# Kernel tuning notes

Measured on AMD Instinct MI355X. Metric: run time of the kernel, lower is better.

Reference implementation:

```python
import jax, jax.numpy as jnp
import numpy as np

N_NODES = 100000
N_EDGES = 1000000  # even: first half = 'in' direction, second half = 'out' (inverse) direction
H = 128
N_REL = 200        # num_relations (for rel_labels embedding)
N_RELG = 100       # num_rel_graph; edge_type in [0, 2*N_RELG)
N_GRAPHS = 256
N_CLS = 2


def _glorot(key, shape):
    s = (6.0 / (shape[0] + shape[1])) ** 0.5
    return jax.random.uniform(key, shape, jnp.float32, -s, s)


def setup_inputs() -> dict:
    key = jax.random.key(0)
    ks = jax.random.split(key, 32)
    inp = {}
    inp['x'] = jax.random.normal(ks[0], (N_NODES, H), jnp.float32)
    inp['edge_index'] = jax.random.randint(ks[1], (2, N_EDGES), 0, N_NODES)
    inp['edge_type'] = jax.random.randint(ks[2], (N_EDGES,), 0, 2 * N_RELG)
    inp['batch'] = jnp.sort(jax.random.randint(ks[3], (N_NODES,), 0, N_GRAPHS))
    inp['rel_labels'] = jax.random.randint(ks[4], (N_GRAPHS,), 0, N_REL)
    inp['drop_prob'] = 0  # eval mode -> dropout is identity
    # learned parameters
    inp['rel_emb_table'] = jax.random.normal(ks[5], (N_REL, H), jnp.float32)
    inp['rel_graph_emb'] = _glorot(ks[6], (N_RELG, H))
    i = 7
    for l in (1, 2, 3):
        for nm in ('w_in', 'w_out', 'w_loop', 'w_rel'):
            inp[f'{nm}{l}'] = _glorot(ks[i], (H, H)); i += 1
        inp[f'loop_rel{l}'] = _glorot(ks[i], (1, H)); i += 1
        inp[f'b{l}'] = jnp.zeros((H,), jnp.float32)
    inp['lin_w'] = _glorot(ks[i], (2 * H, N_CLS))
    inp['lin_b'] = jnp.zeros((N_CLS,), jnp.float32)
    return inp


def _conv(x, edge_index, edge_type, rel, w_in, w_out, w_loop, w_rel, loop_rel, b):
    """CompGCNConv with 'sub' composition, tanh activation (BN/dropout identity in eval)."""
    n = x.shape[0]
    rel_all = jnp.concatenate([rel, loop_rel], axis=0)  # append loop relation
    half = edge_index.shape[1] // 2

    def direction(idx, etyp, w):
        src, dst = idx[0], idx[1]
        # norm as in CompGCN: deg over row(src), norm = deg_inv[row]*deg_inv[col]
        deg = jax.ops.segment_sum(jnp.ones(src.shape[0], x.dtype), src, num_segments=n)
        dinv = jnp.where(deg > 0, deg ** -0.5, 0.0)
        norm = dinv[src] * dinv[dst]                      # [E/2]
        msg = ((x[src] - rel_all[etyp]) @ w) * norm[:, None]  # gather-compose-transform
        return jax.ops.segment_sum(msg, dst, num_segments=n)  # scatter-add

    in_res = direction(edge_index[:, :half], edge_type[:half], w_in)
    out_res = direction(edge_index[:, half:], edge_type[half:], w_out)
    loop_res = (x - rel_all[-1]) @ w_loop
    out = (in_res + out_res + loop_res) * (1.0 / 3.0) + b
    return jnp.tanh(out), (rel_all @ w_rel)[:-1]


def reference(x, rel_emb_table, rel_graph_emb,
              w_in1, w_out1, w_loop1, w_rel1, loop_rel1, b1,
              w_in2, w_out2, w_loop2, w_rel2, loop_rel2, b2,
              w_in3, w_out3, w_loop3, w_rel3, loop_rel3, b3,
              lin_w, lin_b, edge_index, edge_type, batch, rel_labels, drop_prob):
    rel_embs = rel_emb_table[rel_labels]                   # [G, H]
    r = jnp.concatenate([rel_graph_emb, -rel_graph_emb], axis=0)  # [2*N_RELG, H]
    x, r = _conv(x, edge_index, edge_type, r, w_in1, w_out1, w_loop1, w_rel1, loop_rel1, b1)
    x = jax.nn.relu(x)
    x, r = _conv(x, edge_index, edge_type, r, w_in2, w_out2, w_loop2, w_rel2, loop_rel2, b2)
    x = jax.nn.relu(x)
    x, r = _conv(x, edge_index, edge_type, r, w_in3, w_out3, w_loop3, w_rel3, loop_rel3, b3)
    # global mean pool over graphs
    sums = jax.ops.segment_sum(x, batch, num_segments=N_GRAPHS)
    cnt = jax.ops.segment_sum(jnp.ones(batch.shape[0], x.dtype), batch, num_segments=N_GRAPHS)
    x = sums / jnp.maximum(cnt, 1.0)[:, None]              # [G, H]
    x = jnp.concatenate([x, rel_embs], axis=1)             # [G, 2H]
    # dropout identity (eval); final linear
    return x @ lin_w + lin_b                               # [G, 2]
```

## Files before the change

### kernel.cpp

```cpp
#include <hip/hip_runtime.h>
#include <hip/hip_bf16.h>
#include <math.h>

#define N_NODES 100000
#define N_EDGES 1000000
#define HALF_E  500000
#define H       128
#define NG      256
#define RELROWS 201
#define NH      (N_NODES * H)
#define SCAN_NB 98
#define XPITCH  136
#define MMB     64

typedef __attribute__((ext_vector_type(8))) short bf16x8;
typedef __attribute__((ext_vector_type(4))) float f32x4;
typedef __attribute__((ext_vector_type(2))) float f32x2;

__device__ __forceinline__ float bflo(unsigned p) { return __uint_as_float(p << 16); }
__device__ __forceinline__ float bfhi(unsigned p) { return __uint_as_float(p & 0xffff0000u); }
__device__ __forceinline__ unsigned packbf2(float a, float b) {
    unsigned ua = __float_as_uint(a), ub = __float_as_uint(b);
    ua = (ua + 0x7fffu + ((ua >> 16) & 1u)) >> 16;
    ub = (ub + 0x7fffu + ((ub >> 16) & 1u)) >> 16;
    return ua | (ub << 16);
}

__device__ __forceinline__ float fp8_to_f32(unsigned v) {
    unsigned s = (v & 0x80u) << 24;
    float m = __uint_as_float((v & 0x7fu) << 20) * 0x1p+120f;
    return __uint_as_float(__float_as_uint(m) | s);
}

#if __has_builtin(__builtin_amdgcn_cvt_pk_f32_fp8)
__device__ __forceinline__ f32x2 f8pair(unsigned short p) {
    return __builtin_amdgcn_cvt_pk_f32_fp8((int)(unsigned)p, false);
}
#else
__device__ __forceinline__ f32x2 f8pair(unsigned short p) {
    f32x2 r;
    r.x = fp8_to_f32(p & 0xffu);
    r.y = fp8_to_f32((p >> 8) & 0xffu);
    return r;
}
#endif

#if __has_builtin(__builtin_amdgcn_cvt_pk_fp8_f32)
__device__ __forceinline__ unsigned short packfp8_2(float a, float b) {
    int v = __builtin_amdgcn_cvt_pk_fp8_f32(a, b, 0, false);
    return (unsigned short)(v & 0xffff);
}
#else
__device__ __forceinline__ unsigned fp8_enc1(float x) {
    float ax = fabsf(x);
    ax = fminf(ax, 448.f);
    unsigned sgn = (__float_as_uint(x) >> 24) & 0x80u;
    float sc = ax * 0x1p-120f;
    unsigned b = __float_as_uint(sc);
    if (b < 0x00080000u) return sgn;
    unsigned r = b + 0x7ffffu + ((b >> 20) & 1u);
    return sgn | (r >> 20);
}
__device__ __forceinline__ unsigned short packfp8_2(float a, float b) {
    return (unsigned short)(fp8_enc1(a) | (fp8_enc1(b) << 8));
}
#endif

__global__ void deg_hist_kernel(const int* __restrict__ ei, float* deg_in, float* deg_out,
                                int* __restrict__ cnt_dst) {
    int e = blockIdx.x * 256 + threadIdx.x;
    if (e >= N_EDGES) return;
    int src = ei[e];
    int dst = ei[N_EDGES + e];
    if (e < HALF_E) atomicAdd(deg_in + src, 1.0f);
    else            atomicAdd(deg_out + src, 1.0f);
    atomicAdd(cnt_dst + dst, 1);
}

__global__ __launch_bounds__(1024) void scan1_kernel(const int* __restrict__ cnt,
                                                     int* __restrict__ excl,
                                                     int* __restrict__ bsum,
                                                     float* deg_in, float* deg_out) {
    __shared__ int ps[1024];
    int t = threadIdx.x;
    int i = blockIdx.x * 1024 + t;
    if (i < N_NODES) {
        float d = deg_in[i];  deg_in[i]  = d > 0.f ? rsqrtf(d) : 0.f;
        d = deg_out[i];       deg_out[i] = d > 0.f ? rsqrtf(d) : 0.f;
    }
    int v = (i < N_NODES) ? cnt[i] : 0;
    ps[t] = v;
    __syncthreads();
    for (int off = 1; off < 1024; off <<= 1) {
        int u = (t >= off) ? ps[t - off] : 0;
        __syncthreads();
        ps[t] += u;
        __syncthreads();
    }
    if (i < N_NODES) excl[i] = ps[t] - v;
    if (t == 1023) bsum[blockIdx.x] = ps[t];
}

__global__ __launch_bounds__(128) void scan2_kernel(const int* __restrict__ bsum,
                                                    int* __restrict__ boff,
                                                    int* __restrict__ rowptr,
                                                    const int* __restrict__ batch,
                                                    float* __restrict__ cnt_g) {
    __shared__ int ps[128];
    int t = threadIdx.x;
    for (int g = t; g < NG; g += 128) {
        int lo = 0, hi = N_NODES;
        while (lo < hi) { int mid = (lo + hi) >> 1; if (batch[mid] < g) lo = mid + 1; else hi = mid; }
        int start = lo;
        lo = 0; hi = N_NODES;
        while (lo < hi) { int mid = (lo + hi) >> 1; if (batch[mid] < g + 1) lo = mid + 1; else hi = mid; }
        cnt_g[g] = (float)(lo - start);
    }
    int v = (t < SCAN_NB) ? bsum[t] : 0;
    ps[t] = v;
    __syncthreads();
    for (int off = 1; off < 128; off <<= 1) {
        int u = (t >= off) ? ps[t - off] : 0;
        __syncthreads();
        ps[t] += u;
        __syncthreads();
    }
    if (t < SCAN_NB) boff[t] = ps[t] - v;
    if (t == 127) rowptr[N_NODES] = ps[t];
}

__global__ __launch_bounds__(1024) void scan3_kernel(const int* __restrict__ excl,
                                                     const int* __restrict__ boff,
                                                     int* __restrict__ rowptr,
                                                     int* __restrict__ rfill) {
    int t = threadIdx.x;
    int i = blockIdx.x * 1024 + t;
    if (i >= N_NODES) return;
    int r = excl[i] + boff[blockIdx.x];
    rowptr[i] = r;
    rfill[i] = r;
}

__global__ void fill_kernel(const int* __restrict__ ei, const int* __restrict__ etype,
                            const float* __restrict__ dinv_in, const float* __restrict__ dinv_out,
                            int* __restrict__ rfill, int2* __restrict__ csr_mn) {
    int e = blockIdx.x * 256 + threadIdx.x;
    if (e >= N_EDGES) return;
    int s = ei[e], d = ei[N_EDGES + e];
    int t = etype[e];
    bool isin = (e < HALF_E);
    const float* dv = isin ? dinv_in : dinv_out;
    float nv = dv[s] * dv[d];
    int j = atomicAdd(rfill + d, 1);
    int src2 = s + (isin ? 0 : N_NODES);
    int typ2 = t + (isin ? 0 : 200);
    csr_mn[j] = make_int2(src2 | (typ2 << 18), __float_as_int(nv));
}

__global__ void rel_mm_kernel(const float* __restrict__ rge, const float* __restrict__ loop_rel,
                              int layer,
                              const float* __restrict__ wIn, const float* __restrict__ wOut,
                              const float* __restrict__ wRel, const float* __restrict__ wLoop,
                              unsigned short* __restrict__ RWf8, float* __restrict__ rbuf,
                              float* __restrict__ lwl) {
    __shared__ float a[H];
    int i = blockIdx.x, j = threadIdx.x;
    float v;
    if (i == 200)        v = loop_rel[j];
    else if (layer == 1) v = (i < 100) ? rge[i * H + j] : -rge[(i - 100) * H + j];
    else                 v = rbuf[i * H + j];
    a[j] = v;
    __syncthreads();
    float s_in = 0.f, s_out = 0.f, s_rel = 0.f, s_loop = 0.f;
    for (int k = 0; k < H; k++) {
        float av = a[k];
        s_in  += av * wIn [k * H + j];
        s_out += av * wOut[k * H + j];
        s_rel += av * wRel[k * H + j];
        s_loop += av * wLoop[k * H + j];
    }
    float in_n  = __shfl_xor(s_in, 1);
    float out_n = __shfl_xor(s_out, 1);
    if (i < 200) {
        if ((j & 1) == 0) {
            RWf8[i * 64 + (j >> 1)]         = packfp8_2(s_in, in_n);
            RWf8[(200 + i) * 64 + (j >> 1)] = packfp8_2(s_out, out_n);
        }
        rbuf[i * H + j] = s_rel;
    }
    if (i == 200) lwl[j] = s_loop;
}

struct WPtrs { const float* p[9]; };
__global__ __launch_bounds__(256) void wpack_kernel(WPtrs wp, unsigned short* __restrict__ Bp) {
    int iw = blockIdx.y;
    const float* W = wp.p[iw];
    unsigned short* out = Bp + (size_t)iw * 16384;
    int t = blockIdx.x * 256 + threadIdx.x;
    int nt = t >> 8, kk = (t >> 6) & 3, lane = t & 63;
    int n = nt * 16 + (lane & 15);
    int k0 = kk * 32 + (lane >> 4) * 8;
    unsigned p[4];
    for (int j = 0; j < 4; j++)
        p[j] = packbf2(W[(k0 + 2 * j) * H + n], W[(k0 + 2 * j + 1) * H + n]);
    *(uint4*)(out + ((size_t)(nt * 4 + kk) * 64 + lane) * 8) = make_uint4(p[0], p[1], p[2], p[3]);
}

__global__ __launch_bounds__(256) void mm_mfma_kernel(const float* __restrict__ Xf,
                                                      const unsigned short* __restrict__ Xh,
                                                      int xf32,
                                                      const unsigned short* __restrict__ Bpack,
                                                      const float* __restrict__ lwl,
                                                      unsigned short* __restrict__ QRf8,
                                                      unsigned short* __restrict__ Sb) {
    __shared__ unsigned short xt[MMB * XPITCH];
    int tid = threadIdx.x;
    int row0 = blockIdx.x * MMB;
    int nrows = min(MMB, N_NODES - row0);
    if (xf32) {
        for (int t = 0; t < 8; t++) {
            int idx = tid + t * 256;
            int r = idx >> 5, c4 = (idx & 31) * 4;
            if (r < nrows) {
                float4 v = *(const float4*)(Xf + (size_t)(row0 + r) * H + c4);
                *(uint2*)(xt + r * XPITCH + c4) = make_uint2(packbf2(v.x, v.y), packbf2(v.z, v.w));
            }
        }
    } else {
        for (int t = 0; t < 4; t++) {
            int idx = tid + t * 256;
            int r = idx >> 4, c8 = (idx & 15) * 8;
            if (r < nrows)
                *(uint4*)(xt + r * XPITCH + c8) = *(const uint4*)(Xh + (size_t)(row0 + r) * H + c8);
        }
    }
    __syncthreads();

    int wave = tid >> 6, lane = tid & 63;
    int m0w = wave * 16;
    int q = lane >> 4, ml = lane & 15;
    bf16x8 afrag[4];
    for (int kk = 0; kk < 4; kk++)
        afrag[kk] = *(const bf16x8*)(xt + (m0w + ml) * XPITCH + kk * 32 + q * 8);
    __syncthreads();

    if (m0w + 16 > nrows) return;

    unsigned short* stg = xt + wave * 2176;
    unsigned* stg32 = (unsigned*)stg;
    uint4* stg4 = (uint4*)stg;
    int grow0 = row0 + m0w;

    for (int w = 0; w < 3; w++) {
        for (int nt = 0; nt < 8; nt++) {
            const unsigned short* bp = Bpack + (((size_t)(w * 8 + nt) * 4) * 64 + lane) * 8;
            f32x4 acc = {0.f, 0.f, 0.f, 0.f};
            for (int kk = 0; kk < 4; kk++) {
                bf16x8 bfrag = *(const bf16x8*)(bp + (size_t)kk * 512);
                acc = __builtin_amdgcn_mfma_f32_16x16x32_bf16(afrag[kk], bfrag, acc, 0, 0, 0);
            }
            if (w < 2) {
                #pragma unroll
                for (int reg = 0; reg < 4; reg++) {
                    float v = acc[reg];
                    float vn = __shfl_xor(v, 1);
                    if ((lane & 1) == 0)
                        stg[(q * 4 + reg) * 64 + nt * 8 + (ml >> 1)] = packfp8_2(v, vn);
                }
            } else {
                float sub = lwl[nt * 16 + ml];
                #pragma unroll
                for (int reg = 0; reg < 4; reg++) {
                    float v = acc[reg] - sub;
                    float vn = __shfl_xor(v, 1);
                    if ((lane & 1) == 0)
                        stg32[(q * 4 + reg) * 64 + nt * 8 + (ml >> 1)] = packbf2(v, vn);
                }
            }
        }
        if (w < 2) {
            size_t rbase = (w == 0) ? 0 : (size_t)N_NODES;
            uint4* dst = (uint4*)QRf8 + (rbase + grow0) * 8;
            dst[lane]      = stg4[lane];
            dst[lane + 64] = stg4[lane + 64];
        } else {
            uint4* dst = (uint4*)Sb + (size_t)grow0 * 16;
            #pragma unroll
            for (int i = 0; i < 4; i++)
                dst[lane + 64 * i] = stg4[lane + 64 * i];
        }
    }
}

__global__ __launch_bounds__(256, 8) void gather_kernel(const int* __restrict__ rowptr,
                                                        const int2* __restrict__ csr_mn,
                                                        const unsigned short* __restrict__ QRf8,
                                                        const unsigned short* __restrict__ RWf8,
                                                        const float* __restrict__ b,
                                                        unsigned* __restrict__ Sb,
                                                        const int* __restrict__ batch,
                                                        float* __restrict__ pool, int mode) {
    int v = blockIdx.x * 4 + (threadIdx.x >> 6);
    if (v >= N_NODES) return;
    int lane = threadIdx.x & 63;
    int c = lane * 2;
    int jb = rowptr[v], je = rowptr[v + 1];
    unsigned sv = Sb[(size_t)v * 64 + lane];
    float ax = bflo(sv), ay = bfhi(sv);
    int j = jb;
    for (; j + 7 < je; j += 8) {
        int2 mn[8];
        #pragma unroll
        for (int k = 0; k < 8; k++) mn[k] = csr_mn[j + k];
        unsigned short q[8], r[8];
        #pragma unroll
        for (int k = 0; k < 8; k++) {
            q[k] = QRf8[(size_t)(mn[k].x & 0x3FFFF) * 64 + lane];
            r[k] = RWf8[(size_t)((unsigned)mn[k].x >> 18) * 64 + lane];
        }
        #pragma unroll
        for (int k = 0; k < 8; k++) {
            float n = __int_as_float(mn[k].y);
            f32x2 dq = f8pair(q[k]);
            f32x2 dr = f8pair(r[k]);
            ax += (dq.x - dr.x) * n;
            ay += (dq.y - dr.y) * n;
        }
    }
    for (; j + 1 < je; j += 2) {
        int2 mn0 = csr_mn[j], mn1 = csr_mn[j + 1];
        unsigned short q0 = QRf8[(size_t)(mn0.x & 0x3FFFF) * 64 + lane];
        unsigned short r0 = RWf8[(size_t)((unsigned)mn0.x >> 18) * 64 + lane];
        unsigned short q1 = QRf8[(size_t)(mn1.x & 0x3FFFF) * 64 + lane];
        unsigned short r1 = RWf8[(size_t)((unsigned)mn1.x >> 18) * 64 + lane];
        float n0 = __int_as_float(mn0.y), n1 = __int_as_float(mn1.y);
        f32x2 dq0 = f8pair(q0), dr0 = f8pair(r0);
        f32x2 dq1 = f8pair(q1), dr1 = f8pair(r1);
        ax += (dq0.x - dr0.x) * n0; ay += (dq0.y - dr0.y) * n0;
        ax += (dq1.x - dr1.x) * n1; ay += (dq1.y - dr1.y) * n1;
    }
    if (j < je) {
        int2 mn0 = csr_mn[j];
        float n0 = __int_as_float(mn0.y);
        unsigned short q0 = QRf8[(size_t)(mn0.x & 0x3FFFF) * 64 + lane];
        unsigned short r0 = RWf8[(size_t)((unsigned)mn0.x >> 18) * 64 + lane];
        f32x2 dq0 = f8pair(q0), dr0 = f8pair(r0);
        ax += (dq0.x - dr0.x) * n0; ay += (dq0.y - dr0.y) * n0;
    }
    float v0 = tanhf(ax * (1.f / 3.f) + b[c]);
    float v1 = tanhf(ay * (1.f / 3.f) + b[c + 1]);
    if (mode == 0) {
        v0 = fmaxf(v0, 0.f); v1 = fmaxf(v1, 0.f);
        Sb[(size_t)v * 64 + lane] = packbf2(v0, v1);
    } else {
        int g = batch[v];
        atomicAdd(pool + g * H + c,     v0);
        atomicAdd(pool + g * H + c + 1, v1);
    }
}

__global__ void final_kernel(const float* __restrict__ pool, const float* __restrict__ cnt,
                             const float* __restrict__ rel_table, const int* __restrict__ rel_labels,
                             const float* __restrict__ lin_w, const float* __restrict__ lin_b,
                             float* __restrict__ out) {
    int g = blockIdx.x;
    int lane = threadIdx.x;
    float inv = 1.f / fmaxf(cnt[g], 1.f);
    const float* rrow = rel_table + (size_t)rel_labels[g] * H;
    float p0 = 0.f, p1 = 0.f;
    for (int c = lane; c < H; c += 64) {
        float m = pool[g * H + c] * inv;
        p0 += m * lin_w[c * 2 + 0];
        p1 += m * lin_w[c * 2 + 1];
        float rv = rrow[c];
        p0 += rv * lin_w[(H + c) * 2 + 0];
        p1 += rv * lin_w[(H + c) * 2 + 1];
    }
    for (int off = 32; off; off >>= 1) {
        p0 += __shfl_down(p0, off);
        p1 += __shfl_down(p1, off);
    }
    if (lane == 0) {
        out[g * 2 + 0] = p0 + lin_b[0];
        out[g * 2 + 1] = p1 + lin_b[1];
    }
}

extern "C" void kernel_launch(void* const* d_in, const int* in_sizes, int n_in,
                              void* d_out, int out_size, void* d_ws, size_t ws_size,
                              hipStream_t stream) {
    const float* x          = (const float*)d_in[0];
    const int*   ei         = (const int*)  d_in[1];
    const int*   etype      = (const int*)  d_in[2];
    const int*   batch      = (const int*)  d_in[3];
    const int*   rel_labels = (const int*)  d_in[4];
    const float* rel_table  = (const float*)d_in[6];
    const float* rge        = (const float*)d_in[7];
    const float* lin_w      = (const float*)d_in[26];
    const float* lin_b      = (const float*)d_in[27];
    float* out = (float*)d_out;

    float* ws       = (float*)d_ws;
    float* dinv_in  = ws;
    float* dinv_out = dinv_in + N_NODES;
    float* pool     = dinv_out + N_NODES;
    float* cnt      = pool + NG * H;
    float* rbuf     = cnt + NG;
    float* lwl      = rbuf + 200 * H;
    int*   rowptr   = (int*)(lwl + 3 * H);
    int*   rfill    = rowptr + N_NODES + 4;
    int*   cnt_dst  = rfill + N_NODES;
    int*   excl     = cnt_dst + N_NODES;
    int*   bsum     = excl + N_NODES;
    int*   boff     = bsum + 100;
    int2*  csr_mn   = (int2*)(boff + 100);
    unsigned short* QRf8 = (unsigned short*)(csr_mn + N_EDGES);
    unsigned* Sb    = (unsigned*)(QRf8 + (size_t)2 * N_NODES * 64);
    unsigned short* RWf8 = (unsigned short*)(Sb + (size_t)N_NODES * 64);
    unsigned short* Bpack = RWf8 + (size_t)3 * 400 * 64;

    hipMemsetAsync(dinv_in, 0, (size_t)(2 * N_NODES + NG * H + NG) * sizeof(float), stream);
    hipMemsetAsync(cnt_dst, 0, (size_t)N_NODES * sizeof(int), stream);

    deg_hist_kernel<<<(N_EDGES + 255) / 256, 256, 0, stream>>>(ei, dinv_in, dinv_out, cnt_dst);
    scan1_kernel   <<<SCAN_NB, 1024, 0, stream>>>(cnt_dst, excl, bsum, dinv_in, dinv_out);
    scan2_kernel   <<<1, 128, 0, stream>>>(bsum, boff, rowptr, batch, cnt);
    scan3_kernel   <<<SCAN_NB, 1024, 0, stream>>>(excl, boff, rowptr, rfill);
    fill_kernel    <<<(N_EDGES + 255) / 256, 256, 0, stream>>>(ei, etype, dinv_in, dinv_out,
                                                               rfill, csr_mn);

    WPtrs wp;
    for (int l = 0; l < 3; l++) {
        wp.p[l * 3 + 0] = (const float*)d_in[8 + 6 * l + 0];
        wp.p[l * 3 + 1] = (const float*)d_in[8 + 6 * l + 1];
        wp.p[l * 3 + 2] = (const float*)d_in[8 + 6 * l + 2];
    }
    wpack_kernel<<<dim3(8, 9), 256, 0, stream>>>(wp, Bpack);

    for (int l = 0; l < 3; l++) {
        const float* wIn   = (const float*)d_in[8 + 6 * l + 0];
        const float* wOut  = (const float*)d_in[8 + 6 * l + 1];
        const float* wLoop = (const float*)d_in[8 + 6 * l + 2];
        const float* wRel  = (const float*)d_in[8 + 6 * l + 3];
        const float* lrel  = (const float*)d_in[8 + 6 * l + 4];
        rel_mm_kernel<<<RELROWS, H, 0, stream>>>(rge, lrel, l + 1, wIn, wOut, wRel, wLoop,
                                                 RWf8 + (size_t)l * 400 * 64,
                                                 rbuf, lwl + l * H);
    }

    int mm_grid = (N_NODES + MMB - 1) / MMB;
    for (int l = 0; l < 3; l++) {
        const float* bl = (const float*)d_in[8 + 6 * l + 5];
        mm_mfma_kernel<<<mm_grid, 256, 0, stream>>>(x, (const unsigned short*)Sb, (l == 0) ? 1 : 0,
                                                    Bpack + (size_t)l * 3 * 16384, lwl + l * H,
                                                    QRf8, (unsigned short*)Sb);
        gather_kernel<<<N_NODES / 4, 256, 0, stream>>>(rowptr, csr_mn,
                                                       QRf8, RWf8 + (size_t)l * 400 * 64, bl,
                                                       Sb, batch, pool, (l == 2) ? 1 : 0);
    }

    final_kernel<<<NG, 64, 0, stream>>>(pool, cnt, rel_table, rel_labels, lin_w, lin_b, out);
}
```

Measured before the change: 697.1 us.

## Aggregate composed features before the weight transform, then fuse in/out/loop matmuls

The per-layer order changes from transform-then-aggregate to aggregate-then-transform. The gather kernel now reads a single fp8 copy of the node features (N rows instead of 2N precomputed in/out projections), subtracts bf16 relation embeddings, and accumulates separate in- and out-direction sums into bf16 buffers. A new combine kernel then runs MFMA over the in, out and self-loop inputs into one accumulator, and applies bias, tanh, relu and pooling in its epilogue. This halves the randomly gathered table size so it caches better, at the cost of writing and re-reading two extra N×H bf16 aggregate buffers per layer.

Result: slower. 948.4 us (+36.1%).

```diff
diff --git a/kernel.cpp b/kernel.cpp
--- a/kernel.cpp
+++ b/kernel.cpp
@@ -8,7 +8,6 @@
 #define H       128
 #define NG      256
 #define RELROWS 201
-#define NH      (N_NODES * H)
 #define SCAN_NB 98
 #define XPITCH  136
 #define MMB     64
@@ -31,20 +30,15 @@
     float m = __uint_as_float((v & 0x7fu) << 20) * 0x1p+120f;
     return __uint_as_float(__float_as_uint(m) | s);
 }
-
 #if __has_builtin(__builtin_amdgcn_cvt_pk_f32_fp8)
 __device__ __forceinline__ f32x2 f8pair(unsigned short p) {
     return __builtin_amdgcn_cvt_pk_f32_fp8((int)(unsigned)p, false);
 }
 #else
 __device__ __forceinline__ f32x2 f8pair(unsigned short p) {
-    f32x2 r;
-    r.x = fp8_to_f32(p & 0xffu);
-    r.y = fp8_to_f32((p >> 8) & 0xffu);
-    return r;
+    f32x2 r; r.x = fp8_to_f32(p & 0xffu); r.y = fp8_to_f32((p >> 8) & 0xffu); return r;
 }
 #endif
-
 #if __has_builtin(__builtin_amdgcn_cvt_pk_fp8_f32)
 __device__ __forceinline__ unsigned short packfp8_2(float a, float b) {
     int v = __builtin_amdgcn_cvt_pk_fp8_f32(a, b, 0, false);
@@ -152,16 +146,21 @@
     const float* dv = isin ? dinv_in : dinv_out;
     float nv = dv[s] * dv[d];
     int j = atomicAdd(rfill + d, 1);
-    int src2 = s + (isin ? 0 : N_NODES);
-    int typ2 = t + (isin ? 0 : 200);
-    csr_mn[j] = make_int2(src2 | (typ2 << 18), __float_as_int(nv));
+    int m = s | (t << 17) | (isin ? 0 : (1 << 25));
+    csr_mn[j] = make_int2(m, __float_as_int(nv));
+}
+
+__global__ void xcvt_kernel(const float* __restrict__ x, unsigned short* __restrict__ Xf8) {
+    int id = blockIdx.x * 256 + threadIdx.x;
+    if (id >= N_NODES * 64) return;
+    float2 v = *(const float2*)(x + (size_t)id * 2);
+    Xf8[id] = packfp8_2(v.x, v.y);
 }
 
 __global__ void rel_mm_kernel(const float* __restrict__ rge, const float* __restrict__ loop_rel,
                               int layer,
-                              const float* __restrict__ wIn, const float* __restrict__ wOut,
                               const float* __restrict__ wRel, const float* __restrict__ wLoop,
-                              unsigned short* __restrict__ RWf8, float* __restrict__ rbuf,
+                              unsigned* __restrict__ relb, float* __restrict__ rbuf,
                               float* __restrict__ lwl) {
     __shared__ float a[H];
     int i = blockIdx.x, j = threadIdx.x;
@@ -171,23 +170,16 @@
     else                 v = rbuf[i * H + j];
     a[j] = v;
     __syncthreads();
-    float s_in = 0.f, s_out = 0.f, s_rel = 0.f, s_loop = 0.f;
+    float vn = __shfl_xor(v, 1);
+    if (i < 200 && (j & 1) == 0)
+        relb[i * 64 + (j >> 1)] = packbf2(v, vn);
+    float s_rel = 0.f, s_loop = 0.f;
     for (int k = 0; k < H; k++) {
         float av = a[k];
-        s_in  += av * wIn [k * H + j];
-        s_out += av * wOut[k * H + j];
-        s_rel += av * wRel[k * H + j];
+        s_rel  += av * wRel [k * H + j];
         s_loop += av * wLoop[k * H + j];
     }
-    float in_n  = __shfl_xor(s_in, 1);
-    float out_n = __shfl_xor(s_out, 1);
-    if (i < 200) {
-        if ((j & 1) == 0) {
-            RWf8[i * 64 + (j >> 1)]         = packfp8_2(s_in, in_n);
-            RWf8[(200 + i) * 64 + (j >> 1)] = packfp8_2(s_out, out_n);
-        }
-        rbuf[i * H + j] = s_rel;
-    }
+    if (i < 200)  rbuf[i * H + j] = s_rel;
     if (i == 200) lwl[j] = s_loop;
 }
 
@@ -206,24 +198,91 @@
     *(uint4*)(out + ((size_t)(nt * 4 + kk) * 64 + lane) * 8) = make_uint4(p[0], p[1], p[2], p[3]);
 }
 
-__global__ __launch_bounds__(256) void mm_mfma_kernel(const float* __restrict__ Xf,
-                                                      const unsigned short* __restrict__ Xh,
+__global__ __launch_bounds__(256, 8) void gather_kernel(const int* __restrict__ rowptr,
+                                                        const int2* __restrict__ csr_mn,
+                                                        const unsigned short* __restrict__ Xf8,
+                                                        const unsigned* __restrict__ RELb,
+                                                        unsigned* __restrict__ AGGi,
+                                                        unsigned* __restrict__ AGGo) {
+    int v = blockIdx.x * 4 + (threadIdx.x >> 6);
+    if (v >= N_NODES) return;
+    int lane = threadIdx.x & 63;
+    int jb = rowptr[v], je = rowptr[v + 1];
+    float aix = 0.f, aiy = 0.f, aox = 0.f, aoy = 0.f;
+    int j = jb;
+    for (; j + 7 < je; j += 8) {
+        int2 mn[8];
+        #pragma unroll
+        for (int k = 0; k < 8; k++) mn[k] = csr_mn[j + k];
+        unsigned short xq[8]; unsigned rl[8];
+        #pragma unroll
+        for (int k = 0; k < 8; k++) {
+            xq[k] = Xf8[(size_t)(mn[k].x & 0x1FFFF) * 64 + lane];
+            rl[k] = RELb[((mn[k].x >> 17) & 0xFF) * 64 + lane];
+        }
+        #pragma unroll
+        for (int k = 0; k < 8; k++) {
+            float n = __int_as_float(mn[k].y);
+            f32x2 dx = f8pair(xq[k]);
+            float vx = dx.x - bflo(rl[k]);
+            float vy = dx.y - bfhi(rl[k]);
+            bool dir = (mn[k].x >> 25) & 1;
+            float ni = dir ? 0.f : n, no = dir ? n : 0.f;
+            aix += vx * ni; aiy += vy * ni;
+            aox += vx * no; aoy += vy * no;
+        }
+    }
+    for (; j < je; j++) {
+        int2 mn0 = csr_mn[j];
+        float n = __int_as_float(mn0.y);
+        unsigned short xq = Xf8[(size_t)(mn0.x & 0x1FFFF) * 64 + lane];
+        unsigned rl = RELb[((mn0.x >> 17) & 0xFF) * 64 + lane];
+        f32x2 dx = f8pair(xq);
+        float vx = dx.x - bflo(rl);
+        float vy = dx.y - bfhi(rl);
+        bool dir = (mn0.x >> 25) & 1;
+        float ni = dir ? 0.f : n, no = dir ? n : 0.f;
+        aix += vx * ni; aiy += vy * ni;
+        aox += vx * no; aoy += vy * no;
+    }
+    AGGi[(size_t)v * 64 + lane] = packbf2(aix, aiy);
+    AGGo[(size_t)v * 64 + lane] = packbf2(aox, aoy);
+}
+
+__global__ __launch_bounds__(256) void combine_kernel(const float* __restrict__ Xf,
+                                                      const unsigned* __restrict__ Xh,
                                                       int xf32,
+                                                      const unsigned* __restrict__ AGGi,
+                                                      const unsigned* __restrict__ AGGo,
                                                       const unsigned short* __restrict__ Bpack,
                                                       const float* __restrict__ lwl,
-                                                      unsigned short* __restrict__ QRf8,
-                                                      unsigned short* __restrict__ Sb) {
-    __shared__ unsigned short xt[MMB * XPITCH];
+                                                      const float* __restrict__ bvec,
+                                                      unsigned short* __restrict__ Xf8_out,
+                                                      unsigned* __restrict__ Xh_out,
+                                                      const int* __restrict__ batch,
+                                                      float* __restrict__ pool, int mode) {
+    __shared__ unsigned short ti[MMB * XPITCH];
+    __shared__ unsigned short to[MMB * XPITCH];
+    __shared__ unsigned short tx[MMB * XPITCH];
     int tid = threadIdx.x;
     int row0 = blockIdx.x * MMB;
     int nrows = min(MMB, N_NODES - row0);
+
+    for (int t = 0; t < 4; t++) {
+        int idx = tid + t * 256;
+        int r = idx >> 4, c8 = (idx & 15) * 8;
+        if (r < nrows) {
+            *(uint4*)(ti + r * XPITCH + c8) = *(const uint4*)((const unsigned short*)AGGi + (size_t)(row0 + r) * H + c8);
+            *(uint4*)(to + r * XPITCH + c8) = *(const uint4*)((const unsigned short*)AGGo + (size_t)(row0 + r) * H + c8);
+        }
+    }
     if (xf32) {
         for (int t = 0; t < 8; t++) {
             int idx = tid + t * 256;
             int r = idx >> 5, c4 = (idx & 31) * 4;
             if (r < nrows) {
                 float4 v = *(const float4*)(Xf + (size_t)(row0 + r) * H + c4);
-                *(uint2*)(xt + r * XPITCH + c4) = make_uint2(packbf2(v.x, v.y), packbf2(v.z, v.w));
+                *(uint2*)(tx + r * XPITCH + c4) = make_uint2(packbf2(v.x, v.y), packbf2(v.z, v.w));
             }
         }
     } else {
@@ -231,7 +290,7 @@
             int idx = tid + t * 256;
             int r = idx >> 4, c8 = (idx & 15) * 8;
             if (r < nrows)
-                *(uint4*)(xt + r * XPITCH + c8) = *(const uint4*)(Xh + (size_t)(row0 + r) * H + c8);
+                *(uint4*)(tx + r * XPITCH + c8) = *(const uint4*)((const unsigned short*)Xh + (size_t)(row0 + r) * H + c8);
         }
     }
     __syncthreads();
@@ -239,123 +298,69 @@
     int wave = tid >> 6, lane = tid & 63;
     int m0w = wave * 16;
     int q = lane >> 4, ml = lane & 15;
-    bf16x8 afrag[4];
-    for (int kk = 0; kk < 4; kk++)
-        afrag[kk] = *(const bf16x8*)(xt + (m0w + ml) * XPITCH + kk * 32 + q * 8);
+    bf16x8 fi[4], fo[4], fx[4];
+    for (int kk = 0; kk < 4; kk++) {
+        fi[kk] = *(const bf16x8*)(ti + (m0w + ml) * XPITCH + kk * 32 + q * 8);
+        fo[kk] = *(const bf16x8*)(to + (m0w + ml) * XPITCH + kk * 32 + q * 8);
+        fx[kk] = *(const bf16x8*)(tx + (m0w + ml) * XPITCH + kk * 32 + q * 8);
+    }
     __syncthreads();
 
     if (m0w + 16 > nrows) return;
 
-    unsigned short* stg = xt + wave * 2176;
-    unsigned* stg32 = (unsigned*)stg;
-    uint4* stg4 = (uint4*)stg;
     int grow0 = row0 + m0w;
-
-    for (int w = 0; w < 3; w++) {
-        for (int nt = 0; nt < 8; nt++) {
-            const unsigned short* bp = Bpack + (((size_t)(w * 8 + nt) * 4) * 64 + lane) * 8;
-            f32x4 acc = {0.f, 0.f, 0.f, 0.f};
-            for (int kk = 0; kk < 4; kk++) {
-                bf16x8 bfrag = *(const bf16x8*)(bp + (size_t)kk * 512);
-                acc = __builtin_amdgcn_mfma_f32_16x16x32_bf16(afrag[kk], bfrag, acc, 0, 0, 0);
-            }
-            if (w < 2) {
-                #pragma unroll
-                for (int reg = 0; reg < 4; reg++) {
-                    float v = acc[reg];
-                    float vn = __shfl_xor(v, 1);
-                    if ((lane & 1) == 0)
-                        stg[(q * 4 + reg) * 64 + nt * 8 + (ml >> 1)] = packfp8_2(v, vn);
-                }
-            } else {
-                float sub = lwl[nt * 16 + ml];
-                #pragma unroll
-                for (int reg = 0; reg < 4; reg++) {
-                    float v = acc[reg] - sub;
-                    float vn = __shfl_xor(v, 1);
-                    if ((lane & 1) == 0)
-                        stg32[(q * 4 + reg) * 64 + nt * 8 + (ml >> 1)] = packbf2(v, vn);
+    int grow_base = grow0 + q * 4;
+    unsigned short* stg8 = ti + wave * 1024;
+    unsigned* stgh = (unsigned*)to + wave * 1024;
+
+    int gmap[4];
+    if (mode == 1) {
+        #pragma unroll
+        for (int reg = 0; reg < 4; reg++) gmap[reg] = batch[grow_base + reg];
+    }
+
+    for (int nt = 0; nt < 8; nt++) {
+        f32x4 acc = {0.f, 0.f, 0.f, 0.f};
+        const unsigned short* bpI = Bpack + (((size_t)(0 * 8 + nt) * 4) * 64 + lane) * 8;
+        const unsigned short* bpO = Bpack + (((size_t)(1 * 8 + nt) * 4) * 64 + lane) * 8;
+        const unsigned short* bpL = Bpack + (((size_t)(2 * 8 + nt) * 4) * 64 + lane) * 8;
+        for (int kk = 0; kk < 4; kk++)
+            acc = __builtin_amdgcn_mfma_f32_16x16x32_bf16(fi[kk], *(const bf16x8*)(bpI + (size_t)kk * 512), acc, 0, 0, 0);
+        for (int kk = 0; kk < 4; kk++)
+            acc = __builtin_amdgcn_mfma_f32_16x16x32_bf16(fo[kk], *(const bf16x8*)(bpO + (size_t)kk * 512), acc, 0, 0, 0);
+        for (int kk = 0; kk < 4; kk++)
+            acc = __builtin_amdgcn_mfma_f32_16x16x32_bf16(fx[kk], *(const bf16x8*)(bpL + (size_t)kk * 512), acc, 0, 0, 0);
+        int col = nt * 16 + ml;
+        float sub = lwl[col];
+        float bb = bvec[col];
+        if (mode == 0) {
+            #pragma unroll
+            for (int reg = 0; reg < 4; reg++) {
+                float val = fmaxf(tanhf((acc[reg] - sub) * (1.f / 3.f) + bb), 0.f);
+                float vn = __shfl_xor(val, 1);
+                if ((lane & 1) == 0) {
+                    stg8[(q * 4 + reg) * 64 + nt * 8 + (ml >> 1)] = packfp8_2(val, vn);
+                    stgh[(q * 4 + reg) * 64 + nt * 8 + (ml >> 1)] = packbf2(val, vn);
                 }
             }
-        }
-        if (w < 2) {
-            size_t rbase = (w == 0) ? 0 : (size_t)N_NODES;
-            uint4* dst = (uint4*)QRf8 + (rbase + grow0) * 8;
-            dst[lane]      = stg4[lane];
-            dst[lane + 64] = stg4[lane + 64];
         } else {
-            uint4* dst = (uint4*)Sb + (size_t)grow0 * 16;
             #pragma unroll
-            for (int i = 0; i < 4; i++)
-                dst[lane + 64 * i] = stg4[lane + 64 * i];
-        }
-    }
-}
-
-__global__ __launch_bounds__(256, 8) void gather_kernel(const int* __restrict__ rowptr,
-                                                        const int2* __restrict__ csr_mn,
-                                                        const unsigned short* __restrict__ QRf8,
-                                                        const unsigned short* __restrict__ RWf8,
-                                                        const float* __restrict__ b,
-                                                        unsigned* __restrict__ Sb,
-                                                        const int* __restrict__ batch,
-                                                        float* __restrict__ pool, int mode) {
-    int v = blockIdx.x * 4 + (threadIdx.x >> 6);
-    if (v >= N_NODES) return;
-    int lane = threadIdx.x & 63;
-    int c = lane * 2;
-    int jb = rowptr[v], je = rowptr[v + 1];
-    unsigned sv = Sb[(size_t)v * 64 + lane];
-    float ax = bflo(sv), ay = bfhi(sv);
-    int j = jb;
-    for (; j + 7 < je; j += 8) {
-        int2 mn[8];
+            for (int reg = 0; reg < 4; reg++) {
+                float val = tanhf((acc[reg] - sub) * (1.f / 3.f) + bb);
+                atomicAdd(pool + gmap[reg] * H + col, val);
+            }
+        }
+    }
+    if (mode == 0) {
+        uint4* s8 = (uint4*)stg8;
+        uint4* d8 = (uint4*)Xf8_out + (size_t)grow0 * 8;
+        d8[lane]      = s8[lane];
+        d8[lane + 64] = s8[lane + 64];
+        uint4* sh = (uint4*)stgh;
+        uint4* dh = (uint4*)Xh_out + (size_t)grow0 * 16;
         #pragma unroll
-        for (int k = 0; k < 8; k++) mn[k] = csr_mn[j + k];
-        unsigned short q[8], r[8];
-        #pragma unroll
-        for (int k = 0; k < 8; k++) {
-            q[k] = QRf8[(size_t)(mn[k].x & 0x3FFFF) * 64 + lane];
-            r[k] = RWf8[(size_t)((unsigned)mn[k].x >> 18) * 64 + lane];
-        }
-        #pragma unroll
-        for (int k = 0; k < 8; k++) {
-            float n = __int_as_float(mn[k].y);
-            f32x2 dq = f8pair(q[k]);
-            f32x2 dr = f8pair(r[k]);
-            ax += (dq.x - dr.x) * n;
-            ay += (dq.y - dr.y) * n;
-        }
-    }
-    for (; j + 1 < je; j += 2) {
-        int2 mn0 = csr_mn[j], mn1 = csr_mn[j + 1];
-        unsigned short q0 = QRf8[(size_t)(mn0.x & 0x3FFFF) * 64 + lane];
-        unsigned short r0 = RWf8[(size_t)((unsigned)mn0.x >> 18) * 64 + lane];
-        unsigned short q1 = QRf8[(size_t)(mn1.x & 0x3FFFF) * 64 + lane];
-        unsigned short r1 = RWf8[(size_t)((unsigned)mn1.x >> 18) * 64 + lane];
-        float n0 = __int_as_float(mn0.y), n1 = __int_as_float(mn1.y);
-        f32x2 dq0 = f8pair(q0), dr0 = f8pair(r0);
-        f32x2 dq1 = f8pair(q1), dr1 = f8pair(r1);
-        ax += (dq0.x - dr0.x) * n0; ay += (dq0.y - dr0.y) * n0;
-        ax += (dq1.x - dr1.x) * n1; ay += (dq1.y - dr1.y) * n1;
-    }
-    if (j < je) {
-        int2 mn0 = csr_mn[j];
-        float n0 = __int_as_float(mn0.y);
-        unsigned short q0 = QRf8[(size_t)(mn0.x & 0x3FFFF) * 64 + lane];
-        unsigned short r0 = RWf8[(size_t)((unsigned)mn0.x >> 18) * 64 + lane];
-        f32x2 dq0 = f8pair(q0), dr0 = f8pair(r0);
-        ax += (dq0.x - dr0.x) * n0; ay += (dq0.y - dr0.y) * n0;
-    }
-    float v0 = tanhf(ax * (1.f / 3.f) + b[c]);
-    float v1 = tanhf(ay * (1.f / 3.f) + b[c + 1]);
-    if (mode == 0) {
-        v0 = fmaxf(v0, 0.f); v1 = fmaxf(v1, 0.f);
-        Sb[(size_t)v * 64 + lane] = packbf2(v0, v1);
-    } else {
-        int g = batch[v];
-        atomicAdd(pool + g * H + c,     v0);
-        atomicAdd(pool + g * H + c + 1, v1);
+        for (int i = 0; i < 4; i++)
+            dh[lane + 64 * i] = sh[lane + 64 * i];
     }
 }
 
@@ -400,8 +405,14 @@
     const float* lin_b      = (const float*)d_in[27];
     float* out = (float*)d_out;
 
-    float* ws       = (float*)d_ws;
-    float* dinv_in  = ws;
+    int2*  csr_mn = (int2*)d_ws;
+    unsigned short* Xf8 = (unsigned short*)(csr_mn + N_EDGES);
+    unsigned* Xh   = (unsigned*)(Xf8 + (size_t)N_NODES * 64);
+    unsigned* AGGi = Xh + (size_t)N_NODES * 64;
+    unsigned* AGGo = AGGi + (size_t)N_NODES * 64;
+    unsigned* relb = AGGo + (size_t)N_NODES * 64;
+    unsigned short* Bpack = (unsigned short*)(relb + 3 * 200 * 64);
+    float* dinv_in  = (float*)(Bpack + 9 * 16384);
     float* dinv_out = dinv_in + N_NODES;
     float* pool     = dinv_out + N_NODES;
     float* cnt      = pool + NG * H;
@@ -413,11 +424,6 @@
     int*   excl     = cnt_dst + N_NODES;
     int*   bsum     = excl + N_NODES;
     int*   boff     = bsum + 100;
-    int2*  csr_mn   = (int2*)(boff + 100);
-    unsigned short* QRf8 = (unsigned short*)(csr_mn + N_EDGES);
-    unsigned* Sb    = (unsigned*)(QRf8 + (size_t)2 * N_NODES * 64);
-    unsigned short* RWf8 = (unsigned short*)(Sb + (size_t)N_NODES * 64);
-    unsigned short* Bpack = RWf8 + (size_t)3 * 400 * 64;
 
     hipMemsetAsync(dinv_in, 0, (size_t)(2 * N_NODES + NG * H + NG) * sizeof(float), stream);
     hipMemsetAsync(cnt_dst, 0, (size_t)N_NODES * sizeof(int), stream);
@@ -428,6 +434,7 @@
     scan3_kernel   <<<SCAN_NB, 1024, 0, stream>>>(excl, boff, rowptr, rfill);
     fill_kernel    <<<(N_EDGES + 255) / 256, 256, 0, stream>>>(ei, etype, dinv_in, dinv_out,
                                                                rfill, csr_mn);
+    xcvt_kernel    <<<(N_NODES * 64 + 255) / 256, 256, 0, stream>>>(x, Xf8);
 
     WPtrs wp;
     for (int l = 0; l < 3; l++) {
@@ -438,25 +445,25 @@
     wpack_kernel<<<dim3(8, 9), 256, 0, stream>>>(wp, Bpack);
 
     for (int l = 0; l < 3; l++) {
-        const float* wIn   = (const float*)d_in[8 + 6 * l + 0];
-        const float* wOut  = (const float*)d_in[8 + 6 * l + 1];
+        const float* wRel  = (const float*)d_in[8 + 6 * l + 3];
         const float* wLoop = (const float*)d_in[8 + 6 * l + 2];
-        const float* wRel  = (const float*)d_in[8 + 6 * l + 3];
         const float* lrel  = (const float*)d_in[8 + 6 * l + 4];
-        rel_mm_kernel<<<RELROWS, H, 0, stream>>>(rge, lrel, l + 1, wIn, wOut, wRel, wLoop,
-                                                 RWf8 + (size_t)l * 400 * 64,
+        rel_mm_kernel<<<RELROWS, H, 0, stream>>>(rge, lrel, l + 1, wRel, wLoop,
+                                                 relb + (size_t)l * 200 * 64,
                                                  rbuf, lwl + l * H);
     }
 
-    int mm_grid = (N_NODES + MMB - 1) / MMB;
+    int cmb_grid = (N_NODES + MMB - 1) / MMB;
     for (int l = 0; l < 3; l++) {
         const float* bl = (const float*)d_in[8 + 6 * l + 5];
-        mm_mfma_kernel<<<mm_grid, 256, 0, stream>>>(x, (const unsigned short*)Sb, (l == 0) ? 1 : 0,
-                                                    Bpack + (size_t)l * 3 * 16384, lwl + l * H,
-                                                    QRf8, (unsigned short*)Sb);
-        gather_kernel<<<N_NODES / 4, 256, 0, stream>>>(rowptr, csr_mn,
-                                                       QRf8, RWf8 + (size_t)l * 400 * 64, bl,
-                                                       Sb, batch, pool, (l == 2) ? 1 : 0);
+        gather_kernel<<<N_NODES / 4, 256, 0, stream>>>(rowptr, csr_mn, Xf8,
+                                                       relb + (size_t)l * 200 * 64,
+                                                       AGGi, AGGo);
+        combine_kernel<<<cmb_grid, 256, 0, stream>>>(x, Xh, (l == 0) ? 1 : 0,
+                                                     AGGi, AGGo,
+                                                     Bpack + (size_t)l * 3 * 16384,
+                                                     lwl + l * H, bl,
+                                                     Xf8, Xh, batch, pool, (l == 2) ? 1 : 0);
     }
 
     final_kernel<<<NG, 64, 0, stream>>>(pool, cnt, rel_table, rel_labels, lin_w, lin_b, out);
```
